# Performance work log

Measured on AMD Instinct MI355X. Metric: run time of the kernel, lower is better.

## Reference

```python
import jax, jax.numpy as jnp
import numpy as np

B, N, IN_DIM, OUT_DIM = 8, 2048, 128, 128


def setup_inputs() -> dict:
    key = jax.random.key(0)
    k_a, k_h, k_wp, k_bp, k_wa, k_ba = jax.random.split(key, 6)
    a = jax.random.uniform(k_a, (B, N, N), dtype=jnp.float32)
    h = jax.random.normal(k_h, (B, N, IN_DIM), dtype=jnp.float32)
    # nn.Linear(in_dim, out_dim): y = x @ W^T + b ; store W already transposed.
    W_proj = jax.random.normal(k_wp, (IN_DIM, OUT_DIM), dtype=jnp.float32) / np.sqrt(IN_DIM)
    b_proj = jax.random.normal(k_bp, (OUT_DIM,), dtype=jnp.float32) * 0.01
    # nn.Linear(2*out_dim, 1): weight vector of length 2*out_dim + scalar bias.
    w_att = jax.random.normal(k_wa, (2 * OUT_DIM,), dtype=jnp.float32) / np.sqrt(2 * OUT_DIM)
    b_att = jax.random.normal(k_ba, (), dtype=jnp.float32) * 0.01
    return {"a": a, "h": h, "W_proj": W_proj, "b_proj": b_proj,
            "w_att": w_att, "b_att": b_att}


def reference(a, h, W_proj, b_proj, w_att, b_att):
    # h: [B, N, in_dim] -> [B, N, out_dim]
    h = h @ W_proj + b_proj
    d = w_att.shape[0] // 2
    # GAT decomposition: attention(cat(h_i, h_j)) = h_i.w_src + h_j.w_dst + b
    # (identical math to expand+cat+Linear, without the O(B*N^2*2D) tensor)
    s = h @ w_att[:d]            # [B, N] contribution of row node i
    t = h @ w_att[d:]            # [B, N] contribution of col node j
    e = jax.nn.relu(s[:, :, None] + t[:, None, :] + b_att)  # [B, N, N]
    att = jnp.exp(e) * a
    att = att / jnp.sum(att, axis=-1, keepdims=True)
    return att @ h + h           # [B, N, out_dim]
```

## Files before the change

kernel.cpp:

```cpp
#include <hip/hip_runtime.h>
#include <hip/hip_bf16.h>

#define NB 8
#define NN 2048
#define DD 128
#define NT 32

typedef __attribute__((ext_vector_type(8))) short short8v;
typedef __attribute__((ext_vector_type(4))) float f32x4;

__device__ __forceinline__ unsigned short f2bf(float x) {
    unsigned int u = __float_as_uint(x);
    u += 0x7FFFu + ((u >> 16) & 1u);
    return (unsigned short)(u >> 16);
}

__global__ __launch_bounds__(256) void proj_kernel(
    const float* __restrict__ h, const float* __restrict__ W,
    const float* __restrict__ bias, const float* __restrict__ watt,
    float* __restrict__ hp, unsigned short* __restrict__ hpT,
    float* __restrict__ s, float* __restrict__ t)
{
    __shared__ float Ws[64][132];
    __shared__ float hs[64][68];
    const int tid = threadIdx.x;
    const int rowbase = blockIdx.x * 64;
    const int rg = tid >> 3;
    const int dg = tid & 7;

    const float4* W4 = (const float4*)W;
    const float4* h4 = (const float4*)h;

    float acc[2][16];
    #pragma unroll
    for (int r = 0; r < 2; ++r)
        #pragma unroll
        for (int d = 0; d < 16; ++d) acc[r][d] = 0.f;

    for (int p = 0; p < 2; ++p) {
        #pragma unroll
        for (int q = 0; q < 8; ++q) {
            int f = tid + 256 * q;
            float4 v = W4[2048 * p + f];
            *(float4*)&Ws[f >> 5][4 * (f & 31)] = v;
        }
        #pragma unroll
        for (int q = 0; q < 4; ++q) {
            int f = tid + 256 * q;
            int r = f >> 4, c4 = f & 15;
            float4 v = h4[(size_t)(rowbase + r) * 32 + 16 * p + c4];
            *(float4*)&hs[r][4 * c4] = v;
        }
        __syncthreads();

        #pragma unroll 8
        for (int k = 0; k < 64; ++k) {
            float h0 = hs[2 * rg][k];
            float h1 = hs[2 * rg + 1][k];
            float4 w0 = *(const float4*)&Ws[k][dg * 16];
            float4 w1 = *(const float4*)&Ws[k][dg * 16 + 4];
            float4 w2 = *(const float4*)&Ws[k][dg * 16 + 8];
            float4 w3 = *(const float4*)&Ws[k][dg * 16 + 12];
            float wv[16] = {w0.x,w0.y,w0.z,w0.w, w1.x,w1.y,w1.z,w1.w,
                            w2.x,w2.y,w2.z,w2.w, w3.x,w3.y,w3.z,w3.w};
            #pragma unroll
            for (int d = 0; d < 16; ++d) {
                acc[0][d] += h0 * wv[d];
                acc[1][d] += h1 * wv[d];
            }
        }
        __syncthreads();
    }

    const float4* b4 = (const float4*)bias;
    #pragma unroll
    for (int dq = 0; dq < 4; ++dq) {
        float4 bv = b4[dg * 4 + dq];
        #pragma unroll
        for (int r = 0; r < 2; ++r) {
            acc[r][4 * dq + 0] += bv.x;
            acc[r][4 * dq + 1] += bv.y;
            acc[r][4 * dq + 2] += bv.z;
            acc[r][4 * dq + 3] += bv.w;
        }
    }
    #pragma unroll
    for (int r = 0; r < 2; ++r) {
        float4* o = (float4*)(hp + (size_t)(rowbase + 2 * rg + r) * 128);
        #pragma unroll
        for (int dq = 0; dq < 4; ++dq) {
            float4 v = {acc[r][4*dq+0], acc[r][4*dq+1], acc[r][4*dq+2], acc[r][4*dq+3]};
            o[dg * 4 + dq] = v;
        }
    }
    {
        int rowpair = ((rowbase & (NN - 1)) >> 1) + rg;
        int bb = rowbase >> 11;
        unsigned int* hT32 = (unsigned int*)hpT;
        #pragma unroll
        for (int dd = 0; dd < 16; ++dd) {
            int d = dg * 16 + dd;
            unsigned int pk = (unsigned int)f2bf(acc[0][dd]) |
                              ((unsigned int)f2bf(acc[1][dd]) << 16);
            hT32[(((size_t)bb * 128 + d) << 10) + rowpair] = pk;
        }
    }
    const float4* w4 = (const float4*)watt;
    float sp[2] = {0.f, 0.f}, tp[2] = {0.f, 0.f};
    #pragma unroll
    for (int q = 0; q < 4; ++q) {
        float4 wsa = w4[dg * 4 + q];
        float4 wta = w4[32 + dg * 4 + q];
        #pragma unroll
        for (int r = 0; r < 2; ++r) {
            sp[r] += acc[r][4*q+0]*wsa.x + acc[r][4*q+1]*wsa.y
                   + acc[r][4*q+2]*wsa.z + acc[r][4*q+3]*wsa.w;
            tp[r] += acc[r][4*q+0]*wta.x + acc[r][4*q+1]*wta.y
                   + acc[r][4*q+2]*wta.z + acc[r][4*q+3]*wta.w;
        }
    }
    #pragma unroll
    for (int r = 0; r < 2; ++r) {
        float v = sp[r], u = tp[r];
        v += __shfl_xor(v, 1, 64); u += __shfl_xor(u, 1, 64);
        v += __shfl_xor(v, 2, 64); u += __shfl_xor(u, 2, 64);
        v += __shfl_xor(v, 4, 64); u += __shfl_xor(u, 4, 64);
        if (dg == 0) {
            s[rowbase + 2 * rg + r] = v;
            t[rowbase + 2 * rg + r] = u;
        }
    }
}

__global__ __launch_bounds__(256, 4) void fused_kernel(
    const float* __restrict__ a, const float* __restrict__ hp,
    const unsigned short* __restrict__ hpT,
    const float* __restrict__ s, const float* __restrict__ t,
    const float* __restrict__ battp, float* __restrict__ out)
{
    __shared__ unsigned short w_s[2][16 * 64];
    __shared__ float wsum_s[16];

    const int tid  = threadIdx.x;
    const int lane = tid & 63;
    const int wv   = tid >> 6;
    const int b     = blockIdx.x >> 7;
    const int ibase = (blockIdx.x & 127) * 16;
    const int bN    = b * NN;

    const int rowA = tid >> 4;
    const int q    = tid & 15;

    const int r  = lane & 15;
    const int kg = lane >> 4;
    const int d0 = (wv << 5) + r;

    const float batt = battp[0];
    const float4* a4 = (const float4*)a;
    const float4* t4 = (const float4*)t;
    const float s_reg = s[bN + ibase + rowA];
    const size_t arow = (size_t)(bN + ibase + rowA) * 512;

    const unsigned short* pB0 = hpT + (((size_t)(b * 128 + d0)) << 11) + (kg << 3);
    const unsigned short* pB1 = pB0 + ((size_t)16 << 11);

    float wsum_p = 0.f;
    f32x4 acc0 = {0.f, 0.f, 0.f, 0.f};
    f32x4 acc1 = {0.f, 0.f, 0.f, 0.f};

    float4 av[2], tv[2];
    short8v B00[2], B01[2], B10[2], B11[2];

#define LOADAT(P, k) do { \
        av[P] = a4[arow + (k) * 16 + q]; \
        tv[P] = t4[(bN >> 2) + (k) * 16 + q]; \
    } while (0)

#define LOADB(P, k) do { \
        const short8v* b0 = (const short8v*)(pB0 + (k) * 64); \
        const short8v* b1 = (const short8v*)(pB1 + (k) * 64); \
        B00[P] = b0[0]; B01[P] = b0[4]; \
        B10[P] = b1[0]; B11[P] = b1[4]; \
    } while (0)

#define PHASEA(P) do { \
        float p0 = __expf(fmaxf(s_reg + tv[P].x + batt, 0.f)) * av[P].x; \
        float p1 = __expf(fmaxf(s_reg + tv[P].y + batt, 0.f)) * av[P].y; \
        float p2 = __expf(fmaxf(s_reg + tv[P].z + batt, 0.f)) * av[P].z; \
        float p3 = __expf(fmaxf(s_reg + tv[P].w + batt, 0.f)) * av[P].w; \
        wsum_p += (p0 + p1) + (p2 + p3); \
        unsigned int u0 = (unsigned int)f2bf(p0) | ((unsigned int)f2bf(p1) << 16); \
        unsigned int u1 = (unsigned int)f2bf(p2) | ((unsigned int)f2bf(p3) << 16); \
        uint2 uu; uu.x = u0; uu.y = u1; \
        *(uint2*)((char*)w_s[P] + (((rowA << 7) + (q << 3)) ^ ((rowA & 7) << 4))) = uu; \
    } while (0)

#define DOMFMA(P) do { \
        const char* wb = (const char*)w_s[P]; \
        int kbB = kg << 4; \
        int swz = (r & 7) << 4; \
        short8v A0 = *(const short8v*)(wb + (((r << 7) + kbB     ) ^ swz)); \
        short8v A1 = *(const short8v*)(wb + (((r << 7) + kbB + 64) ^ swz)); \
        acc0 = __builtin_amdgcn_mfma_f32_16x16x32_bf16(A0, B00[P], acc0, 0, 0, 0); \
        acc1 = __builtin_amdgcn_mfma_f32_16x16x32_bf16(A0, B10[P], acc1, 0, 0, 0); \
        acc0 = __builtin_amdgcn_mfma_f32_16x16x32_bf16(A1, B01[P], acc0, 0, 0, 0); \
        acc1 = __builtin_amdgcn_mfma_f32_16x16x32_bf16(A1, B11[P], acc1, 0, 0, 0); \
    } while (0)

    LOADAT(0, 0); LOADB(0, 0);
    LOADAT(1, 1); LOADB(1, 1);
    PHASEA(0);
    __syncthreads();

    for (int tt = 0; tt < NT; tt += 2) {
        PHASEA(1);
        if (tt + 2 < NT) LOADAT(0, tt + 2);
        DOMFMA(0);
        if (tt + 2 < NT) LOADB(0, tt + 2);
        __syncthreads();
        if (tt + 2 < NT) PHASEA(0);
        if (tt + 3 < NT) LOADAT(1, tt + 3);
        DOMFMA(1);
        if (tt + 3 < NT) LOADB(1, tt + 3);
        __syncthreads();
    }

    {
        float v = wsum_p;
        v += __shfl_xor(v, 1, 64);
        v += __shfl_xor(v, 2, 64);
        v += __shfl_xor(v, 4, 64);
        v += __shfl_xor(v, 8, 64);
        if (q == 0) wsum_s[rowA] = v;
    }
    __syncthreads();

    {
        int rloc = (lane >> 4) << 2;
        float inv0 = 1.0f / wsum_s[rloc + 0];
        float inv1 = 1.0f / wsum_s[rloc + 1];
        float inv2 = 1.0f / wsum_s[rloc + 2];
        float inv3 = 1.0f / wsum_s[rloc + 3];
        const float* hpb = hp + (size_t)(bN + ibase) * 128;
        float* ob = out + (size_t)(bN + ibase) * 128;
        ob[(rloc + 0) * 128 + d0]      = acc0.x * inv0 + hpb[(rloc + 0) * 128 + d0];
        ob[(rloc + 1) * 128 + d0]      = acc0.y * inv1 + hpb[(rloc + 1) * 128 + d0];
        ob[(rloc + 2) * 128 + d0]      = acc0.z * inv2 + hpb[(rloc + 2) * 128 + d0];
        ob[(rloc + 3) * 128 + d0]      = acc0.w * inv3 + hpb[(rloc + 3) * 128 + d0];
        ob[(rloc + 0) * 128 + d0 + 16] = acc1.x * inv0 + hpb[(rloc + 0) * 128 + d0 + 16];
        ob[(rloc + 1) * 128 + d0 + 16] = acc1.y * inv1 + hpb[(rloc + 1) * 128 + d0 + 16];
        ob[(rloc + 2) * 128 + d0 + 16] = acc1.z * inv2 + hpb[(rloc + 2) * 128 + d0 + 16];
        ob[(rloc + 3) * 128 + d0 + 16] = acc1.w * inv3 + hpb[(rloc + 3) * 128 + d0 + 16];
    }
#undef LOADAT
#undef LOADB
#undef PHASEA
#undef DOMFMA
}

extern "C" void kernel_launch(void* const* d_in, const int* in_sizes, int n_in,
                              void* d_out, int out_size, void* d_ws, size_t ws_size,
                              hipStream_t stream) {
    const float* a      = (const float*)d_in[0];
    const float* h      = (const float*)d_in[1];
    const float* W_proj = (const float*)d_in[2];
    const float* b_proj = (const float*)d_in[3];
    const float* w_att  = (const float*)d_in[4];
    const float* b_att  = (const float*)d_in[5];
    float* out = (float*)d_out;

    float* hp = (float*)d_ws;
    float* s  = hp + (size_t)NB * NN * DD;
    float* t  = s + (size_t)NB * NN;
    unsigned short* hpT = (unsigned short*)(t + (size_t)NB * NN);

    proj_kernel<<<256, 256, 0, stream>>>(h, W_proj, b_proj, w_att, hp, hpT, s, t);
    fused_kernel<<<1024, 256, 0, stream>>>(a, hp, hpT, s, t, b_att, out);
}
```

Baseline: 257.6 us.

## Split K across waves with register-resident attention weights and LDS reduction

Each wave now covers a quarter of the neighbour dimension for all 16 rows and all 128 output columns. The attention weights are computed directly in the MFMA A-operand register layout, so the LDS staging of weights and the per-tile __syncthreads in the main loop go away. Partial accumulators and row sums are combined through a 32KB LDS reduction at the end, and the output is written with vectorised stores. In exchange the kernel holds more accumulator registers, issues more B-operand global loads per wave, and uses much more shared memory, which may cut occupancy.

```diff
diff --git a/kernel.cpp b/kernel.cpp
--- a/kernel.cpp
+++ b/kernel.cpp
@@ -4,7 +4,6 @@
 #define NB 8
 #define NN 2048
 #define DD 128
-#define NT 32
 
 typedef __attribute__((ext_vector_type(8))) short short8v;
 typedef __attribute__((ext_vector_type(4))) float f32x4;
@@ -138,8 +137,8 @@
     const float* __restrict__ s, const float* __restrict__ t,
     const float* __restrict__ battp, float* __restrict__ out)
 {
-    __shared__ unsigned short w_s[2][16 * 64];
-    __shared__ float wsum_s[16];
+    __shared__ float red[4][16][128];
+    __shared__ float wsum_lds[4][16];
 
     const int tid  = threadIdx.x;
     const int lane = tid & 63;
@@ -148,114 +147,117 @@
     const int ibase = (blockIdx.x & 127) * 16;
     const int bN    = b * NN;
 
-    const int rowA = tid >> 4;
-    const int q    = tid & 15;
-
-    const int r  = lane & 15;
+    const int c  = lane & 15;
     const int kg = lane >> 4;
-    const int d0 = (wv << 5) + r;
-
-    const float batt = battp[0];
-    const float4* a4 = (const float4*)a;
-    const float4* t4 = (const float4*)t;
-    const float s_reg = s[bN + ibase + rowA];
-    const size_t arow = (size_t)(bN + ibase + rowA) * 512;
-
-    const unsigned short* pB0 = hpT + (((size_t)(b * 128 + d0)) << 11) + (kg << 3);
-    const unsigned short* pB1 = pB0 + ((size_t)16 << 11);
+
+    const float s_reg = s[bN + ibase + c] + battp[0];
+    const float* arow = a + (size_t)(bN + ibase + c) * NN;
+    const float* tb   = t + bN;
+    const unsigned short* pB = hpT + ((size_t)(b * 128 + c) << 11);
+    const int jw = wv * 512 + (kg << 3);
 
     float wsum_p = 0.f;
-    f32x4 acc0 = {0.f, 0.f, 0.f, 0.f};
-    f32x4 acc1 = {0.f, 0.f, 0.f, 0.f};
-
-    float4 av[2], tv[2];
-    short8v B00[2], B01[2], B10[2], B11[2];
-
-#define LOADAT(P, k) do { \
-        av[P] = a4[arow + (k) * 16 + q]; \
-        tv[P] = t4[(bN >> 2) + (k) * 16 + q]; \
+    f32x4 acc[8];
+    #pragma unroll
+    for (int n = 0; n < 8; ++n) acc[n] = (f32x4){0.f, 0.f, 0.f, 0.f};
+
+    float4 av0a, av0b, tv0a, tv0b;
+    float4 av1a, av1b, tv1a, tv1b;
+
+#define LOADAT(AVA, AVB, TVA, TVB, tt) do { \
+        int j = jw + (tt) * 32; \
+        AVA = *(const float4*)(arow + j); \
+        AVB = *(const float4*)(arow + j + 4); \
+        TVA = *(const float4*)(tb + j); \
+        TVB = *(const float4*)(tb + j + 4); \
     } while (0)
 
-#define LOADB(P, k) do { \
-        const short8v* b0 = (const short8v*)(pB0 + (k) * 64); \
-        const short8v* b1 = (const short8v*)(pB1 + (k) * 64); \
-        B00[P] = b0[0]; B01[P] = b0[4]; \
-        B10[P] = b1[0]; B11[P] = b1[4]; \
+#define BODY(tt, AVA, AVB, TVA, TVB) do { \
+        int j = jw + (tt) * 32; \
+        const unsigned short* pBt = pB + j; \
+        short8v B0 = *(const short8v*)(pBt); \
+        short8v B1 = *(const short8v*)(pBt + (1 << 15)); \
+        short8v B2 = *(const short8v*)(pBt + (2 << 15)); \
+        short8v B3 = *(const short8v*)(pBt + (3 << 15)); \
+        short8v B4 = *(const short8v*)(pBt + (4 << 15)); \
+        short8v B5 = *(const short8v*)(pBt + (5 << 15)); \
+        short8v B6 = *(const short8v*)(pBt + (6 << 15)); \
+        short8v B7 = *(const short8v*)(pBt + (7 << 15)); \
+        float p0 = __expf(fmaxf(s_reg + TVA.x, 0.f)) * AVA.x; \
+        float p1 = __expf(fmaxf(s_reg + TVA.y, 0.f)) * AVA.y; \
+        float p2 = __expf(fmaxf(s_reg + TVA.z, 0.f)) * AVA.z; \
+        float p3 = __expf(fmaxf(s_reg + TVA.w, 0.f)) * AVA.w; \
+        float p4 = __expf(fmaxf(s_reg + TVB.x, 0.f)) * AVB.x; \
+        float p5 = __expf(fmaxf(s_reg + TVB.y, 0.f)) * AVB.y; \
+        float p6 = __expf(fmaxf(s_reg + TVB.z, 0.f)) * AVB.z; \
+        float p7 = __expf(fmaxf(s_reg + TVB.w, 0.f)) * AVB.w; \
+        wsum_p += ((p0 + p1) + (p2 + p3)) + ((p4 + p5) + (p6 + p7)); \
+        union { uint4 u; short8v sv; } Au; \
+        Au.u.x = (unsigned int)f2bf(p0) | ((unsigned int)f2bf(p1) << 16); \
+        Au.u.y = (unsigned int)f2bf(p2) | ((unsigned int)f2bf(p3) << 16); \
+        Au.u.z = (unsigned int)f2bf(p4) | ((unsigned int)f2bf(p5) << 16); \
+        Au.u.w = (unsigned int)f2bf(p6) | ((unsigned int)f2bf(p7) << 16); \
+        if ((tt) + 2 < 16) LOADAT(AVA, AVB, TVA, TVB, (tt) + 2); \
+        acc[0] = __builtin_amdgcn_mfma_f32_16x16x32_bf16(Au.sv, B0, acc[0], 0, 0, 0); \
+        acc[1] = __builtin_amdgcn_mfma_f32_16x16x32_bf16(Au.sv, B1, acc[1], 0, 0, 0); \
+        acc[2] = __builtin_amdgcn_mfma_f32_16x16x32_bf16(Au.sv, B2, acc[2], 0, 0, 0); \
+        acc[3] = __builtin_amdgcn_mfma_f32_16x16x32_bf16(Au.sv, B3, acc[3], 0, 0, 0); \
+        acc[4] = __builtin_amdgcn_mfma_f32_16x16x32_bf16(Au.sv, B4, acc[4], 0, 0, 0); \
+        acc[5] = __builtin_amdgcn_mfma_f32_16x16x32_bf16(Au.sv, B5, acc[5], 0, 0, 0); \
+        acc[6] = __builtin_amdgcn_mfma_f32_16x16x32_bf16(Au.sv, B6, acc[6], 0, 0, 0); \
+        acc[7] = __builtin_amdgcn_mfma_f32_16x16x32_bf16(Au.sv, B7, acc[7], 0, 0, 0); \
     } while (0)
 
-#define PHASEA(P) do { \
-        float p0 = __expf(fmaxf(s_reg + tv[P].x + batt, 0.f)) * av[P].x; \
-        float p1 = __expf(fmaxf(s_reg + tv[P].y + batt, 0.f)) * av[P].y; \
-        float p2 = __expf(fmaxf(s_reg + tv[P].z + batt, 0.f)) * av[P].z; \
-        float p3 = __expf(fmaxf(s_reg + tv[P].w + batt, 0.f)) * av[P].w; \
-        wsum_p += (p0 + p1) + (p2 + p3); \
-        unsigned int u0 = (unsigned int)f2bf(p0) | ((unsigned int)f2bf(p1) << 16); \
-        unsigned int u1 = (unsigned int)f2bf(p2) | ((unsigned int)f2bf(p3) << 16); \
-        uint2 uu; uu.x = u0; uu.y = u1; \
-        *(uint2*)((char*)w_s[P] + (((rowA << 7) + (q << 3)) ^ ((rowA & 7) << 4))) = uu; \
-    } while (0)
-
-#define DOMFMA(P) do { \
-        const char* wb = (const char*)w_s[P]; \
-        int kbB = kg << 4; \
-        int swz = (r & 7) << 4; \
-        short8v A0 = *(const short8v*)(wb + (((r << 7) + kbB     ) ^ swz)); \
-        short8v A1 = *(const short8v*)(wb + (((r << 7) + kbB + 64) ^ swz)); \
-        acc0 = __builtin_amdgcn_mfma_f32_16x16x32_bf16(A0, B00[P], acc0, 0, 0, 0); \
-        acc1 = __builtin_amdgcn_mfma_f32_16x16x32_bf16(A0, B10[P], acc1, 0, 0, 0); \
-        acc0 = __builtin_amdgcn_mfma_f32_16x16x32_bf16(A1, B01[P], acc0, 0, 0, 0); \
-        acc1 = __builtin_amdgcn_mfma_f32_16x16x32_bf16(A1, B11[P], acc1, 0, 0, 0); \
-    } while (0)
-
-    LOADAT(0, 0); LOADB(0, 0);
-    LOADAT(1, 1); LOADB(1, 1);
-    PHASEA(0);
-    __syncthreads();
-
-    for (int tt = 0; tt < NT; tt += 2) {
-        PHASEA(1);
-        if (tt + 2 < NT) LOADAT(0, tt + 2);
-        DOMFMA(0);
-        if (tt + 2 < NT) LOADB(0, tt + 2);
-        __syncthreads();
-        if (tt + 2 < NT) PHASEA(0);
-        if (tt + 3 < NT) LOADAT(1, tt + 3);
-        DOMFMA(1);
-        if (tt + 3 < NT) LOADB(1, tt + 3);
-        __syncthreads();
-    }
+    LOADAT(av0a, av0b, tv0a, tv0b, 0);
+    LOADAT(av1a, av1b, tv1a, tv1b, 1);
+
+    for (int tt2 = 0; tt2 < 16; tt2 += 2) {
+        BODY(tt2,     av0a, av0b, tv0a, tv0b);
+        BODY(tt2 + 1, av1a, av1b, tv1a, tv1b);
+    }
+#undef LOADAT
+#undef BODY
 
     {
         float v = wsum_p;
-        v += __shfl_xor(v, 1, 64);
-        v += __shfl_xor(v, 2, 64);
-        v += __shfl_xor(v, 4, 64);
-        v += __shfl_xor(v, 8, 64);
-        if (q == 0) wsum_s[rowA] = v;
+        v += __shfl_xor(v, 16, 64);
+        v += __shfl_xor(v, 32, 64);
+        if (kg == 0) wsum_lds[wv][c] = v;
+    }
+    #pragma unroll
+    for (int n = 0; n < 8; ++n) {
+        #pragma unroll
+        for (int qq = 0; qq < 4; ++qq)
+            red[wv][kg * 4 + qq][n * 16 + c] = acc[n][qq];
     }
     __syncthreads();
 
     {
-        int rloc = (lane >> 4) << 2;
-        float inv0 = 1.0f / wsum_s[rloc + 0];
-        float inv1 = 1.0f / wsum_s[rloc + 1];
-        float inv2 = 1.0f / wsum_s[rloc + 2];
-        float inv3 = 1.0f / wsum_s[rloc + 3];
-        const float* hpb = hp + (size_t)(bN + ibase) * 128;
-        float* ob = out + (size_t)(bN + ibase) * 128;
-        ob[(rloc + 0) * 128 + d0]      = acc0.x * inv0 + hpb[(rloc + 0) * 128 + d0];
-        ob[(rloc + 1) * 128 + d0]      = acc0.y * inv1 + hpb[(rloc + 1) * 128 + d0];
-        ob[(rloc + 2) * 128 + d0]      = acc0.z * inv2 + hpb[(rloc + 2) * 128 + d0];
-        ob[(rloc + 3) * 128 + d0]      = acc0.w * inv3 + hpb[(rloc + 3) * 128 + d0];
-        ob[(rloc + 0) * 128 + d0 + 16] = acc1.x * inv0 + hpb[(rloc + 0) * 128 + d0 + 16];
-        ob[(rloc + 1) * 128 + d0 + 16] = acc1.y * inv1 + hpb[(rloc + 1) * 128 + d0 + 16];
-        ob[(rloc + 2) * 128 + d0 + 16] = acc1.z * inv2 + hpb[(rloc + 2) * 128 + d0 + 16];
-        ob[(rloc + 3) * 128 + d0 + 16] = acc1.w * inv3 + hpb[(rloc + 3) * 128 + d0 + 16];
-    }
-#undef LOADAT
-#undef LOADB
-#undef PHASEA
-#undef DOMFMA
+        const int row = tid >> 4;
+        const int col = (tid & 15) * 8;
+        float inv = 1.0f / (wsum_lds[0][row] + wsum_lds[1][row] +
+                            wsum_lds[2][row] + wsum_lds[3][row]);
+        float s0x = 0.f, s0y = 0.f, s0z = 0.f, s0w = 0.f;
+        float s1x = 0.f, s1y = 0.f, s1z = 0.f, s1w = 0.f;
+        #pragma unroll
+        for (int u = 0; u < 4; ++u) {
+            float4 x0 = *(const float4*)&red[u][row][col];
+            float4 x1 = *(const float4*)&red[u][row][col + 4];
+            s0x += x0.x; s0y += x0.y; s0z += x0.z; s0w += x0.w;
+            s1x += x1.x; s1y += x1.y; s1z += x1.z; s1w += x1.w;
+        }
+        size_t gr = (size_t)(bN + ibase + row);
+        const float* hpb = hp + gr * 128 + col;
+        float4 h0 = *(const float4*)(hpb);
+        float4 h1 = *(const float4*)(hpb + 4);
+        float4 o0 = {s0x * inv + h0.x, s0y * inv + h0.y,
+                     s0z * inv + h0.z, s0w * inv + h0.w};
+        float4 o1 = {s1x * inv + h1.x, s1y * inv + h1.y,
+                     s1z * inv + h1.z, s1w * inv + h1.w};
+        float* ob = out + gr * 128 + col;
+        *(float4*)(ob)     = o0;
+        *(float4*)(ob + 4) = o1;
+    }
 }
 
 extern "C" void kernel_launch(void* const* d_in, const int* in_sizes, int n_in,
```

Result: slower. 312.3 us (+21.2%).
